# Performance work log

Hardware: AMD Instinct MI355X
Metric: run time of the kernel (lower is better)

Reference implementation:

```python
import jax, jax.numpy as jnp
import numpy as np

N_SEG, N_REG, N_EDGE, HID, CHEB_K = 40000, 1000, 640000, 256, 5


def setup_inputs() -> dict:
    key = jax.random.key(0)
    ks = jax.random.split(key, 6)
    return {
        "projected_region_features": jax.random.normal(ks[0], (N_REG, HID), jnp.float32),
        "segment2region_assignment": jax.random.uniform(ks[1], (N_SEG, N_REG), jnp.float32),
        "edge_index": jax.random.randint(ks[2], (2, N_EDGE), 0, N_SEG, dtype=jnp.int64),
        # ChebConv params: one [HID,HID] weight per Chebyshev order + shared bias
        "cheb_W": jax.random.normal(ks[3], (CHEB_K, HID, HID), jnp.float32) / np.sqrt(HID).astype(np.float32),
        "cheb_b": jnp.zeros((HID,), jnp.float32),
        "ln_gamma": jnp.ones((HID,), jnp.float32),
        "ln_beta": jnp.zeros((HID,), jnp.float32),
    }


def _cheb_conv(x, edge_index, W, b):
    """PyG ChebConv with normalization='sym', lambda_max=2.0.
    Scaled Laplacian L_hat = 2L/lam - I = -D^{-1/2} A D^{-1/2} (diag = 0)."""
    N = x.shape[0]
    src, dst = edge_index[0], edge_index[1]
    w = (src != dst).astype(x.dtype)  # remove_self_loops
    deg = jax.ops.segment_sum(w, src, num_segments=N)
    dinv = jnp.where(deg > 0, jax.lax.rsqrt(jnp.where(deg > 0, deg, 1.0)), 0.0)
    norm = -w * dinv[src] * dinv[dst]  # per-edge weight of L_hat

    def prop(t):  # y_i = sum_{(j->i)} norm_e * t_j
        return jax.ops.segment_sum(norm[:, None] * t[src], dst, num_segments=N)

    Tx0 = x
    out = Tx0 @ W[0]
    Tx1 = prop(Tx0)
    out = out + Tx1 @ W[1]
    for k in range(2, W.shape[0]):
        Tx2 = 2.0 * prop(Tx1) - Tx0
        out = out + Tx2 @ W[k]
        Tx0, Tx1 = Tx1, Tx2
    return out + b


def _layer_norm(x, g, b, eps=1e-5):
    mu = jnp.mean(x, axis=-1, keepdims=True)
    var = jnp.mean(jnp.square(x - mu), axis=-1, keepdims=True)
    return (x - mu) * jax.lax.rsqrt(var + eps) * g + b


def reference(projected_region_features, segment2region_assignment, edge_index,
              cheb_W, cheb_b, ln_gamma, ln_beta):
    # [n_seg, n_reg] @ [n_reg, hid] -> [n_seg, hid]
    seg_low_raw = segment2region_assignment @ projected_region_features
    seg_low = _cheb_conv(seg_low_raw, edge_index, cheb_W, cheb_b)
    seg_low = _layer_norm(jax.nn.gelu(seg_low, approximate=False), ln_gamma, ln_beta)
    return (seg_low, seg_low_raw)
```

## Files before the change

kernel.cpp:

```cpp
#include <hip/hip_runtime.h>

#define NSEG 40000
#define NREG 1000
#define NEDGE 640000
#define HID 256
#define KCAT 1280
#define KP1 1024
#define LPAD 40
#define NBLK 157

typedef float f32x4 __attribute__((ext_vector_type(4)));
typedef short s16x8 __attribute__((ext_vector_type(8)));
typedef unsigned short u16x4 __attribute__((ext_vector_type(4)));
typedef unsigned short u16x8 __attribute__((ext_vector_type(8)));

typedef __attribute__((address_space(3))) unsigned int lds_u32;
typedef __attribute__((address_space(1))) const unsigned int glb_u32;

__device__ __forceinline__ void dma16(const void* g, void* l) {
    __builtin_amdgcn_global_load_lds((glb_u32*)g, (lds_u32*)l, 16, 0, 0);
}

__device__ __forceinline__ unsigned short f2bf(float f) {
    unsigned u = __builtin_bit_cast(unsigned, f);
    u += 0x7FFFu + ((u >> 16) & 1u);
    return (unsigned short)(u >> 16);
}
__device__ __forceinline__ float bf2f(unsigned short h) {
    unsigned u = ((unsigned)h) << 16;
    return __builtin_bit_cast(float, u);
}

__device__ __forceinline__ f32x4 mfma16(s16x8 a, s16x8 b, f32x4 c) {
    return __builtin_amdgcn_mfma_f32_16x16x32_bf16(a, b, c, 0, 0, 0);
}

__global__ void detect_kernel(const unsigned int* __restrict__ E, int* flag) {
    int lane = threadIdx.x;
    unsigned v = E[2 * lane + 1];
    unsigned long long m = __ballot(v == 0u);
    if (lane == 0) *flag = (__popcll(m) >= 48) ? 1 : 0;
}

__device__ __forceinline__ int edge_at(const void* E, int idx, int is64) {
    return is64 ? (int)((const long long*)E)[idx] : ((const int*)E)[idx];
}

__global__ __launch_bounds__(256) void deg_cnt_kernel(const void* __restrict__ E,
                                                      const int* __restrict__ flag,
                                                      int* deg, int* cnt) {
    int e = blockIdx.x * 256 + threadIdx.x;
    if (e >= NEDGE) return;
    int is64 = *flag;
    int s = edge_at(E, e, is64);
    int d = edge_at(E, e + NEDGE, is64);
    if (s != d) {
        atomicAdd(&deg[s], 1);
        atomicAdd(&cnt[d], 1);
    }
}

__global__ __launch_bounds__(256) void dinv_kernel(const int* __restrict__ deg,
                                                   float* __restrict__ dinv) {
    int i = blockIdx.x * 256 + threadIdx.x;
    if (i < NSEG) {
        int d = deg[i];
        dinv[i] = d > 0 ? rsqrtf((float)d) : 0.f;
    }
}

__global__ __launch_bounds__(256) void scan1_kernel(const int* __restrict__ cnt,
                                                    int* __restrict__ bsum) {
    __shared__ int sh[256];
    int t = threadIdx.x;
    int i = blockIdx.x * 256 + t;
    sh[t] = (i < NSEG) ? cnt[i] : 0;
    __syncthreads();
    for (int o = 128; o > 0; o >>= 1) {
        if (t < o) sh[t] += sh[t + o];
        __syncthreads();
    }
    if (t == 0) bsum[blockIdx.x] = sh[0];
}

__global__ __launch_bounds__(256) void scan2_kernel(const int* __restrict__ bsum,
                                                    int* __restrict__ boff,
                                                    int* __restrict__ rowptr) {
    __shared__ int sh[256];
    int t = threadIdx.x;
    int v = (t < NBLK) ? bsum[t] : 0;
    sh[t] = v;
    __syncthreads();
    for (int o = 1; o < 256; o <<= 1) {
        int x = 0;
        if (t >= o) x = sh[t - o];
        __syncthreads();
        if (t >= o) sh[t] += x;
        __syncthreads();
    }
    if (t < NBLK) boff[t] = sh[t] - v;
    if (t == 255) rowptr[NSEG] = sh[255];
}

__global__ __launch_bounds__(256) void scan3_kernel(const int* __restrict__ cnt,
                                                    const int* __restrict__ boff,
                                                    int* __restrict__ rowptr,
                                                    int* __restrict__ cursor) {
    __shared__ int sh[256];
    int t = threadIdx.x;
    int i = blockIdx.x * 256 + t;
    int v = (i < NSEG) ? cnt[i] : 0;
    sh[t] = v;
    __syncthreads();
    for (int o = 1; o < 256; o <<= 1) {
        int x = 0;
        if (t >= o) x = sh[t - o];
        __syncthreads();
        if (t >= o) sh[t] += x;
        __syncthreads();
    }
    if (i < NSEG) {
        int p = boff[blockIdx.x] + sh[t] - v;
        rowptr[i] = p;
        cursor[i] = p;
    }
}

__global__ __launch_bounds__(256) void scatter_kernel(const void* __restrict__ E,
                                                      const int* __restrict__ flag,
                                                      const float* __restrict__ dinv,
                                                      int* cursor,
                                                      int* __restrict__ colidx,
                                                      float* __restrict__ val) {
    int e = blockIdx.x * 256 + threadIdx.x;
    if (e >= NEDGE) return;
    int is64 = *flag;
    int s = edge_at(E, e, is64);
    int d = edge_at(E, e + NEDGE, is64);
    if (s != d) {
        int pos = atomicAdd(&cursor[d], 1);
        colidx[pos] = s;
        val[pos] = -dinv[s] * dinv[d];
    }
}

__global__ void prep_pt_kernel(const float* __restrict__ P, unsigned short* __restrict__ Pt) {
    int n = blockIdx.x;
    for (int k = threadIdx.x; k < KP1; k += blockDim.x)
        Pt[(size_t)n * KP1 + k] = (k < NREG) ? f2bf(P[(size_t)k * HID + n]) : (unsigned short)0;
}
__global__ void prep_wt_kernel(const float* __restrict__ W, unsigned short* __restrict__ Wt) {
    int n = blockIdx.x;
    for (int k = threadIdx.x; k < KCAT; k += blockDim.x)
        Wt[(size_t)n * KCAT + k] = f2bf(W[(size_t)k * HID + n]);
}

__global__ __launch_bounds__(256) void gemm1_kernel(const float* __restrict__ S,
                                                    const unsigned short* __restrict__ Pt,
                                                    float* __restrict__ raw,
                                                    unsigned short* __restrict__ xcat) {
    __shared__ unsigned short As[64][LPAD];
    __shared__ unsigned short Bs[256][LPAD];
    const int m0 = blockIdx.x * 64;
    const int tid = threadIdx.x;
    const int lane = tid & 63, wn = tid >> 6;
    const int r = lane & 15, q = lane >> 4;
    const int srow = tid >> 2, scol = (tid & 3) * 8;

    f32x4 acc[4][4] = {};

    for (int kb = 0; kb < NREG; kb += 32) {
        const bool kvalid = (kb + scol + 8 <= NREG);
        u16x8 av = {0, 0, 0, 0, 0, 0, 0, 0};
        u16x8 bv0 = av, bv1 = av, bv2 = av, bv3 = av;
        if (kvalid) {
            const float* sp = S + (size_t)(m0 + srow) * NREG + kb + scol;
            f32x4 f0 = *(const f32x4*)sp;
            f32x4 f1 = *(const f32x4*)(sp + 4);
            av[0] = f2bf(f0[0]); av[1] = f2bf(f0[1]); av[2] = f2bf(f0[2]); av[3] = f2bf(f0[3]);
            av[4] = f2bf(f1[0]); av[5] = f2bf(f1[1]); av[6] = f2bf(f1[2]); av[7] = f2bf(f1[3]);
            bv0 = *(const u16x8*)(Pt + (size_t)(srow)       * KP1 + kb + scol);
            bv1 = *(const u16x8*)(Pt + (size_t)(srow +  64) * KP1 + kb + scol);
            bv2 = *(const u16x8*)(Pt + (size_t)(srow + 128) * KP1 + kb + scol);
            bv3 = *(const u16x8*)(Pt + (size_t)(srow + 192) * KP1 + kb + scol);
        }
        __syncthreads();
        *(u16x8*)&As[srow][scol] = av;
        *(u16x8*)&Bs[srow][scol] = bv0;
        *(u16x8*)&Bs[srow + 64][scol] = bv1;
        *(u16x8*)&Bs[srow + 128][scol] = bv2;
        *(u16x8*)&Bs[srow + 192][scol] = bv3;
        __syncthreads();
        s16x8 af[4], bfv[4];
#pragma unroll
        for (int am = 0; am < 4; ++am) af[am] = *(const s16x8*)&As[am * 16 + r][q * 8];
#pragma unroll
        for (int bn = 0; bn < 4; ++bn) bfv[bn] = *(const s16x8*)&Bs[wn * 64 + bn * 16 + r][q * 8];
#pragma unroll
        for (int am = 0; am < 4; ++am) {
#pragma unroll
            for (int bn = 0; bn < 4; ++bn)
                acc[am][bn] = mfma16(af[am], bfv[bn], acc[am][bn]);
        }
    }
#pragma unroll
    for (int am = 0; am < 4; ++am) {
        int rowb = m0 + am * 16 + q * 4;
#pragma unroll
        for (int bn = 0; bn < 4; ++bn) {
            int col = wn * 64 + bn * 16 + r;
#pragma unroll
            for (int i = 0; i < 4; ++i) {
                float v = acc[am][bn][i];
                raw[(size_t)(rowb + i) * HID + col] = v;
                xcat[(size_t)(rowb + i) * KCAT + col] = f2bf(v);
            }
        }
    }
}

__global__ __launch_bounds__(256) void prop_kernel(unsigned short* xcat,
                                                   const int* __restrict__ rowptr,
                                                   const int* __restrict__ colidx,
                                                   const float* __restrict__ val,
                                                   int inOff, int outOff, int subOff,
                                                   float scale) {
    int g = blockIdx.x * 4 + (threadIdx.x >> 6);
    int lane = threadIdx.x & 63;
    int e0 = rowptr[g], e1 = rowptr[g + 1];
    float a0 = 0.f, a1 = 0.f, a2 = 0.f, a3 = 0.f;
    const unsigned short* xin = xcat + inOff + lane * 4;
    for (int base = e0; base < e1; base += 64) {
        int m = e1 - base;
        if (m > 64) m = 64;
        int cc = 0;
        float vv = 0.f;
        if (lane < m) {
            cc = colidx[base + lane];
            vv = val[base + lane];
        }
        int i = 0;
        for (; i + 8 <= m; i += 8) {
            u16x4 t[8];
#pragma unroll
            for (int j = 0; j < 8; ++j) {
                int c = __shfl(cc, i + j);
                t[j] = *(const u16x4*)(xin + (size_t)c * KCAT);
            }
#pragma unroll
            for (int j = 0; j < 8; ++j) {
                float v = __shfl(vv, i + j);
                a0 += v * bf2f(t[j][0]);
                a1 += v * bf2f(t[j][1]);
                a2 += v * bf2f(t[j][2]);
                a3 += v * bf2f(t[j][3]);
            }
        }
        for (; i < m; ++i) {
            int c = __shfl(cc, i);
            float v = __shfl(vv, i);
            u16x4 t = *(const u16x4*)(xin + (size_t)c * KCAT);
            a0 += v * bf2f(t[0]);
            a1 += v * bf2f(t[1]);
            a2 += v * bf2f(t[2]);
            a3 += v * bf2f(t[3]);
        }
    }
    a0 *= scale; a1 *= scale; a2 *= scale; a3 *= scale;
    if (subOff >= 0) {
        u16x4 p = *(const u16x4*)(xcat + (size_t)g * KCAT + subOff + lane * 4);
        a0 -= bf2f(p[0]); a1 -= bf2f(p[1]); a2 -= bf2f(p[2]); a3 -= bf2f(p[3]);
    }
    u16x4 o = {f2bf(a0), f2bf(a1), f2bf(a2), f2bf(a3)};
    *(u16x4*)(xcat + (size_t)g * KCAT + outOff + lane * 4) = o;
}

__global__ __launch_bounds__(512) void gemm2_kernel(const unsigned short* __restrict__ xcat,
                                                    const unsigned short* __restrict__ Wt,
                                                    const float* __restrict__ bias,
                                                    const float* __restrict__ gamma,
                                                    const float* __restrict__ beta,
                                                    float* __restrict__ outp) {
    __shared__ unsigned short As[2][128 * 32];
    __shared__ unsigned short Bs[2][256 * 32];
    __shared__ float rs[128][4];
    __shared__ float rss[128][4];
    const int tid = threadIdx.x;
    const int lane = tid & 63, wid = tid >> 6;
    const int wm = wid >> 2, wn = wid & 3;
    const int r = lane & 15, q = lane >> 4;
    const int qx8 = (q ^ (r & 3)) << 3;
    const int m0 = blockIdx.x * 128;
    const int crow = lane >> 2;
    const int bcol = (((lane & 3) ^ ((lane >> 2) & 3)) << 3);

    f32x4 acc[4][4] = {};

    auto stage = [&](int c, int kb) {
#pragma unroll
        for (int k = 0; k < 3; ++k) {
            int idx = 3 * wid + k;
            if (idx < 16) {
                int n = idx * 16 + crow;
                dma16(Wt + (size_t)n * KCAT + kb + bcol, &Bs[c][idx * 512]);
            } else {
                int a = idx - 16;
                int row = m0 + a * 16 + crow;
                dma16(xcat + (size_t)row * KCAT + kb + bcol, &As[c][a * 512]);
            }
        }
    };

    stage(0, 0);
    __syncthreads();

    for (int t = 0; t < 40; ++t) {
        const int c = t & 1;
        if (t < 39) stage(c ^ 1, (t + 1) * 32);
        s16x8 af[4], bfv[4];
#pragma unroll
        for (int am = 0; am < 4; ++am)
            af[am] = *(const s16x8*)&As[c][(wm * 64 + am * 16 + r) * 32 + qx8];
#pragma unroll
        for (int bn = 0; bn < 4; ++bn)
            bfv[bn] = *(const s16x8*)&Bs[c][(wn * 64 + bn * 16 + r) * 32 + qx8];
#pragma unroll
        for (int am = 0; am < 4; ++am)
#pragma unroll
            for (int bn = 0; bn < 4; ++bn)
                acc[am][bn] = mfma16(af[am], bfv[bn], acc[am][bn]);
        __syncthreads();
    }

    float bc[4], gm[4], bt[4];
#pragma unroll
    for (int bn = 0; bn < 4; ++bn) {
        int col = wn * 64 + bn * 16 + r;
        bc[bn] = bias[col];
        gm[bn] = gamma[col];
        bt[bn] = beta[col];
    }
#pragma unroll
    for (int am = 0; am < 4; ++am) {
#pragma unroll
        for (int i = 0; i < 4; ++i) {
            float s = 0.f, ss = 0.f;
#pragma unroll
            for (int bn = 0; bn < 4; ++bn) {
                float v = acc[am][bn][i] + bc[bn];
                v = 0.5f * v * (1.f + erff(v * 0.70710678118654752f));
                acc[am][bn][i] = v;
                s += v;
                ss += v * v;
            }
#pragma unroll
            for (int msk = 1; msk < 16; msk <<= 1) {
                s += __shfl_xor(s, msk);
                ss += __shfl_xor(ss, msk);
            }
            if (r == 0) {
                int row = wm * 64 + am * 16 + q * 4 + i;
                rs[row][wn] = s;
                rss[row][wn] = ss;
            }
        }
    }
    __syncthreads();
#pragma unroll
    for (int am = 0; am < 4; ++am) {
#pragma unroll
        for (int i = 0; i < 4; ++i) {
            int row = wm * 64 + am * 16 + q * 4 + i;
            float s = rs[row][0] + rs[row][1] + rs[row][2] + rs[row][3];
            float ss = rss[row][0] + rss[row][1] + rss[row][2] + rss[row][3];
            float mu = s * (1.f / HID);
            float var = ss * (1.f / HID) - mu * mu;
            float inv = rsqrtf(var + 1e-5f);
            if (m0 + row < NSEG) {
#pragma unroll
                for (int bn = 0; bn < 4; ++bn) {
                    int col = wn * 64 + bn * 16 + r;
                    outp[(size_t)(m0 + row) * HID + col] = (acc[am][bn][i] - mu) * inv * gm[bn] + bt[bn];
                }
            }
        }
    }
}

extern "C" void kernel_launch(void* const* d_in, const int* in_sizes, int n_in,
                              void* d_out, int out_size, void* d_ws, size_t ws_size,
                              hipStream_t stream) {
    const float* P     = (const float*)d_in[0];
    const float* S     = (const float*)d_in[1];
    const void*  E     = d_in[2];
    const float* W     = (const float*)d_in[3];
    const float* bias  = (const float*)d_in[4];
    const float* gamma = (const float*)d_in[5];
    const float* beta  = (const float*)d_in[6];

    float* out = (float*)d_out;
    float* raw = out + (size_t)NSEG * HID;

    char* ws = (char*)d_ws;
    size_t off = 0;
    auto alloc = [&](size_t bytes) -> void* {
        void* p = ws + off;
        off += (bytes + 255) & ~(size_t)255;
        return p;
    };
    unsigned short* xcat   = (unsigned short*)alloc((size_t)NSEG * KCAT * 2);
    unsigned short* Pt     = (unsigned short*)alloc((size_t)HID * KP1 * 2);
    unsigned short* Wt     = (unsigned short*)alloc((size_t)HID * KCAT * 2);
    int*            deg    = (int*)alloc((size_t)NSEG * 4);
    float*          dinv   = (float*)alloc((size_t)NSEG * 4);
    int*            cnt    = (int*)alloc((size_t)NSEG * 4);
    int*            rowptr = (int*)alloc((size_t)(NSEG + 1) * 4);
    int*            cursor = (int*)alloc((size_t)NSEG * 4);
    int*            colidx = (int*)alloc((size_t)NEDGE * 4);
    float*          val    = (float*)alloc((size_t)NEDGE * 4);
    int*            bsum   = (int*)alloc((size_t)NBLK * 4);
    int*            boff   = (int*)alloc((size_t)NBLK * 4);
    int*            flag   = (int*)alloc(256);
    if (off > ws_size) return;

    hipMemsetAsync(deg, 0, (size_t)NSEG * 4, stream);
    hipMemsetAsync(cnt, 0, (size_t)NSEG * 4, stream);

    detect_kernel<<<1, 64, 0, stream>>>((const unsigned int*)E, flag);
    prep_pt_kernel<<<HID, 256, 0, stream>>>(P, Pt);
    prep_wt_kernel<<<HID, 256, 0, stream>>>(W, Wt);

    deg_cnt_kernel<<<NEDGE / 256, 256, 0, stream>>>(E, flag, deg, cnt);
    dinv_kernel<<<(NSEG + 255) / 256, 256, 0, stream>>>(deg, dinv);
    scan1_kernel<<<NBLK, 256, 0, stream>>>(cnt, bsum);
    scan2_kernel<<<1, 256, 0, stream>>>(bsum, boff, rowptr);
    scan3_kernel<<<NBLK, 256, 0, stream>>>(cnt, boff, rowptr, cursor);
    scatter_kernel<<<NEDGE / 256, 256, 0, stream>>>(E, flag, dinv, cursor, colidx, val);

    gemm1_kernel<<<NSEG / 64, 256, 0, stream>>>(S, Pt, raw, xcat);

    prop_kernel<<<NSEG / 4, 256, 0, stream>>>(xcat, rowptr, colidx, val, 0 * HID, 1 * HID, -1, 1.f);
    prop_kernel<<<NSEG / 4, 256, 0, stream>>>(xcat, rowptr, colidx, val, 1 * HID, 2 * HID, 0 * HID, 2.f);
    prop_kernel<<<NSEG / 4, 256, 0, stream>>>(xcat, rowptr, colidx, val, 2 * HID, 3 * HID, 1 * HID, 2.f);
    prop_kernel<<<NSEG / 4, 256, 0, stream>>>(xcat, rowptr, colidx, val, 3 * HID, 4 * HID, 2 * HID, 2.f);

    gemm2_kernel<<<(NSEG + 127) / 128, 512, 0, stream>>>(xcat, Wt, bias, gamma, beta, out);
}
```

Baseline: 436.8 us.

## Pack CSR col/val into 64-bit entries and split SpMM columns across passes

The scatter stage now stores each edge's source index and normalized weight as one 64-bit word, replacing two separate arrays so each edge needs a single load. The propagation kernel is re-partitioned: every block handles one 64-column slice of four rows, with one bf16 element per lane instead of four, and the grid grows fourfold. This is meant to raise parallelism and the number of gathers in flight for the memory-bound sparse propagation. In exchange, each row's CSR entries are read four times, and each gather is now a 2-byte access per lane instead of 8 bytes, which may waste memory bandwidth.

Result: slower. 567.6 us (+29.9%).

```diff
diff --git a/kernel.cpp b/kernel.cpp
--- a/kernel.cpp
+++ b/kernel.cpp
@@ -130,8 +130,7 @@
                                                       const int* __restrict__ flag,
                                                       const float* __restrict__ dinv,
                                                       int* cursor,
-                                                      int* __restrict__ colidx,
-                                                      float* __restrict__ val) {
+                                                      long long* __restrict__ colval) {
     int e = blockIdx.x * 256 + threadIdx.x;
     if (e >= NEDGE) return;
     int is64 = *flag;
@@ -139,8 +138,9 @@
     int d = edge_at(E, e + NEDGE, is64);
     if (s != d) {
         int pos = atomicAdd(&cursor[d], 1);
-        colidx[pos] = s;
-        val[pos] = -dinv[s] * dinv[d];
+        float v = -dinv[s] * dinv[d];
+        colval[pos] = ((long long)(unsigned)__builtin_bit_cast(unsigned, v) << 32)
+                    | (unsigned)s;
     }
 }
 
@@ -221,58 +221,63 @@
 
 __global__ __launch_bounds__(256) void prop_kernel(unsigned short* xcat,
                                                    const int* __restrict__ rowptr,
-                                                   const int* __restrict__ colidx,
-                                                   const float* __restrict__ val,
+                                                   const long long* __restrict__ colval,
                                                    int inOff, int outOff, int subOff,
                                                    float scale) {
-    int g = blockIdx.x * 4 + (threadIdx.x >> 6);
-    int lane = threadIdx.x & 63;
+    const int bid = blockIdx.x;
+    const int pass = bid / (NSEG / 4);
+    const int ng   = bid % (NSEG / 4);
+    const int g = ng * 4 + (threadIdx.x >> 6);
+    const int lane = threadIdx.x & 63;
+    const int col = pass * 64 + lane;
+    const unsigned short* xin = xcat + inOff + col;
     int e0 = rowptr[g], e1 = rowptr[g + 1];
-    float a0 = 0.f, a1 = 0.f, a2 = 0.f, a3 = 0.f;
-    const unsigned short* xin = xcat + inOff + lane * 4;
+    float a = 0.f;
     for (int base = e0; base < e1; base += 64) {
         int m = e1 - base;
         if (m > 64) m = 64;
         int cc = 0;
         float vv = 0.f;
         if (lane < m) {
-            cc = colidx[base + lane];
-            vv = val[base + lane];
+            long long cv = colval[base + lane];
+            cc = (int)(unsigned)cv;
+            vv = __builtin_bit_cast(float, (unsigned)(cv >> 32));
         }
         int i = 0;
         for (; i + 8 <= m; i += 8) {
-            u16x4 t[8];
-#pragma unroll
-            for (int j = 0; j < 8; ++j) {
-                int c = __shfl(cc, i + j);
-                t[j] = *(const u16x4*)(xin + (size_t)c * KCAT);
-            }
-#pragma unroll
-            for (int j = 0; j < 8; ++j) {
-                float v = __shfl(vv, i + j);
-                a0 += v * bf2f(t[j][0]);
-                a1 += v * bf2f(t[j][1]);
-                a2 += v * bf2f(t[j][2]);
-                a3 += v * bf2f(t[j][3]);
-            }
+            float t0, t1, t2, t3, t4, t5, t6, t7;
+            {
+                int c0 = __shfl(cc, i + 0), c1 = __shfl(cc, i + 1);
+                int c2 = __shfl(cc, i + 2), c3 = __shfl(cc, i + 3);
+                int c4 = __shfl(cc, i + 4), c5 = __shfl(cc, i + 5);
+                int c6 = __shfl(cc, i + 6), c7 = __shfl(cc, i + 7);
+                t0 = bf2f(xin[(size_t)c0 * KCAT]);
+                t1 = bf2f(xin[(size_t)c1 * KCAT]);
+                t2 = bf2f(xin[(size_t)c2 * KCAT]);
+                t3 = bf2f(xin[(size_t)c3 * KCAT]);
+                t4 = bf2f(xin[(size_t)c4 * KCAT]);
+                t5 = bf2f(xin[(size_t)c5 * KCAT]);
+                t6 = bf2f(xin[(size_t)c6 * KCAT]);
+                t7 = bf2f(xin[(size_t)c7 * KCAT]);
+            }
+            a += __shfl(vv, i + 0) * t0;
+            a += __shfl(vv, i + 1) * t1;
+            a += __shfl(vv, i + 2) * t2;
+            a += __shfl(vv, i + 3) * t3;
+            a += __shfl(vv, i + 4) * t4;
+            a += __shfl(vv, i + 5) * t5;
+            a += __shfl(vv, i + 6) * t6;
+            a += __shfl(vv, i + 7) * t7;
         }
         for (; i < m; ++i) {
             int c = __shfl(cc, i);
             float v = __shfl(vv, i);
-            u16x4 t = *(const u16x4*)(xin + (size_t)c * KCAT);
-            a0 += v * bf2f(t[0]);
-            a1 += v * bf2f(t[1]);
-            a2 += v * bf2f(t[2]);
-            a3 += v * bf2f(t[3]);
-        }
-    }
-    a0 *= scale; a1 *= scale; a2 *= scale; a3 *= scale;
-    if (subOff >= 0) {
-        u16x4 p = *(const u16x4*)(xcat + (size_t)g * KCAT + subOff + lane * 4);
-        a0 -= bf2f(p[0]); a1 -= bf2f(p[1]); a2 -= bf2f(p[2]); a3 -= bf2f(p[3]);
-    }
-    u16x4 o = {f2bf(a0), f2bf(a1), f2bf(a2), f2bf(a3)};
-    *(u16x4*)(xcat + (size_t)g * KCAT + outOff + lane * 4) = o;
+            a += v * bf2f(xin[(size_t)c * KCAT]);
+        }
+    }
+    a *= scale;
+    if (subOff >= 0) a -= bf2f(xcat[(size_t)g * KCAT + subOff + col]);
+    xcat[(size_t)g * KCAT + outOff + col] = f2bf(a);
 }
 
 __global__ __launch_bounds__(512) void gemm2_kernel(const unsigned short* __restrict__ xcat,
@@ -416,8 +421,7 @@
     int*            cnt    = (int*)alloc((size_t)NSEG * 4);
     int*            rowptr = (int*)alloc((size_t)(NSEG + 1) * 4);
     int*            cursor = (int*)alloc((size_t)NSEG * 4);
-    int*            colidx = (int*)alloc((size_t)NEDGE * 4);
-    float*          val    = (float*)alloc((size_t)NEDGE * 4);
+    long long*      colval = (long long*)alloc((size_t)NEDGE * 8);
     int*            bsum   = (int*)alloc((size_t)NBLK * 4);
     int*            boff   = (int*)alloc((size_t)NBLK * 4);
     int*            flag   = (int*)alloc(256);
@@ -435,14 +439,14 @@
     scan1_kernel<<<NBLK, 256, 0, stream>>>(cnt, bsum);
     scan2_kernel<<<1, 256, 0, stream>>>(bsum, boff, rowptr);
     scan3_kernel<<<NBLK, 256, 0, stream>>>(cnt, boff, rowptr, cursor);
-    scatter_kernel<<<NEDGE / 256, 256, 0, stream>>>(E, flag, dinv, cursor, colidx, val);
+    scatter_kernel<<<NEDGE / 256, 256, 0, stream>>>(E, flag, dinv, cursor, colval);
 
     gemm1_kernel<<<NSEG / 64, 256, 0, stream>>>(S, Pt, raw, xcat);
 
-    prop_kernel<<<NSEG / 4, 256, 0, stream>>>(xcat, rowptr, colidx, val, 0 * HID, 1 * HID, -1, 1.f);
-    prop_kernel<<<NSEG / 4, 256, 0, stream>>>(xcat, rowptr, colidx, val, 1 * HID, 2 * HID, 0 * HID, 2.f);
-    prop_kernel<<<NSEG / 4, 256, 0, stream>>>(xcat, rowptr, colidx, val, 2 * HID, 3 * HID, 1 * HID, 2.f);
-    prop_kernel<<<NSEG / 4, 256, 0, stream>>>(xcat, rowptr, colidx, val, 3 * HID, 4 * HID, 2 * HID, 2.f);
+    prop_kernel<<<NSEG, 256, 0, stream>>>(xcat, rowptr, colval, 0 * HID, 1 * HID, -1, 1.f);
+    prop_kernel<<<NSEG, 256, 0, stream>>>(xcat, rowptr, colval, 1 * HID, 2 * HID, 0 * HID, 2.f);
+    prop_kernel<<<NSEG, 256, 0, stream>>>(xcat, rowptr, colval, 2 * HID, 3 * HID, 1 * HID, 2.f);
+    prop_kernel<<<NSEG, 256, 0, stream>>>(xcat, rowptr, colval, 3 * HID, 4 * HID, 2 * HID, 2.f);
 
     gemm2_kernel<<<(NSEG + 127) / 128, 512, 0, stream>>>(xcat, Wt, bias, gamma, beta, out);
 }
```
